# Performance work log

Hardware: AMD Instinct MI355X
Metric: run time of the kernel (lower is better)

## Reference

```python
import jax, jax.numpy as jnp
import numpy as np

EPS = 1e-5

def layer_norm(x, gamma, beta):
    m = jnp.mean(x, axis=-1, keepdims=True)
    v = jnp.var(x, axis=-1, keepdims=True)
    return (x - m) * jax.lax.rsqrt(v + EPS) * gamma + beta


def setup_inputs() -> dict:
    key = jax.random.key(0)
    ks = jax.random.split(key, 8)
    B, N, E, C = 1, 512, 128, 128
    s = 0.02
    inp = {
        "pair_rep": jax.random.normal(ks[0], (B, N, N, E), dtype=jnp.float32),
        "ln_pair_g": jnp.ones((E,), jnp.float32),
        "ln_pair_b": jnp.zeros((E,), jnp.float32),
        "ga_w": jax.random.normal(ks[1], (E, C), jnp.float32) * s,
        "ga_b": jnp.zeros((C,), jnp.float32),
        "la_w": jax.random.normal(ks[2], (E, C), jnp.float32) * s,
        "la_b": jnp.zeros((C,), jnp.float32),
        "gb_w": jax.random.normal(ks[3], (E, C), jnp.float32) * s,
        "gb_b": jnp.zeros((C,), jnp.float32),
        "lb_w": jax.random.normal(ks[4], (E, C), jnp.float32) * s,
        "lb_b": jnp.zeros((C,), jnp.float32),
        "g_w": jax.random.normal(ks[5], (E, E), jnp.float32) * s,
        "g_b": jnp.zeros((E,), jnp.float32),
        "ln_up_g": jnp.ones((C,), jnp.float32),
        "ln_up_b": jnp.zeros((C,), jnp.float32),
        "lu_w": jax.random.normal(ks[6], (C, E), jnp.float32) * s,
        "lu_b": jnp.zeros((E,), jnp.float32),
    }
    return inp


def reference(pair_rep, ln_pair_g, ln_pair_b, ga_w, ga_b, la_w, la_b,
              gb_w, gb_b, lb_w, lb_b, g_w, g_b, ln_up_g, ln_up_b, lu_w, lu_b):
    # pair_rep: [B, N, N, E]
    z = layer_norm(pair_rep, ln_pair_g, ln_pair_b)
    a = jax.nn.sigmoid(z @ ga_w + ga_b) * (z @ la_w + la_b)  # [B,N,N,C]
    b = jax.nn.sigmoid(z @ gb_w + gb_b) * (z @ lb_w + lb_b)  # [B,N,N,C]
    g = jax.nn.sigmoid(z @ g_w + g_b)                        # [B,N,N,E]
    # torch: sum(a.unsqueeze(-3)*b.unsqueeze(-4), dim=-2) == sum_k a[i,k,c]*b[j,k,c]
    update = jnp.einsum("bikc,bjkc->bijc", a, b)             # [B,N,N,C]
    out = g * (layer_norm(update, ln_up_g, ln_up_b) @ lu_w + lu_b)
    return out
```

## Files before the change

kernel.cpp:

```cpp
#include <hip/hip_runtime.h>
#include <hip/hip_bf16.h>

#define NN 512
#define MM (NN*NN)

typedef __attribute__((ext_vector_type(8))) unsigned short u16x8;
typedef __attribute__((ext_vector_type(4))) unsigned short u16x4;
typedef __attribute__((ext_vector_type(8))) __bf16 bf16x8;
typedef __attribute__((ext_vector_type(4))) float f32x4;

static __device__ __forceinline__ unsigned short f2bfi(float f) {
  return __builtin_bit_cast(unsigned short, __float2bfloat16(f));
}
static __device__ __forceinline__ float bf2f(unsigned short h) {
  return __uint_as_float(((unsigned int)h) << 16);
}
static __device__ __forceinline__ bf16x8 ldfrag(const unsigned short* p) {
  u16x8 v = *(const u16x8*)p;
  return __builtin_bit_cast(bf16x8, v);
}
static __device__ __forceinline__ float sigm(float x) {
  return 1.0f / (1.0f + __expf(-x));
}

__global__ void prep_weights(const float* __restrict__ ga_w, const float* __restrict__ la_w,
                             const float* __restrict__ gb_w, const float* __restrict__ lb_w,
                             const float* __restrict__ g_w,  const float* __restrict__ lu_w,
                             unsigned short* __restrict__ WT) {
  int idx = blockIdx.x * 256 + threadIdx.x;
  if (idx >= 768 * 128) return;
  int n = idx >> 7;
  int k = idx & 127;
  int grp = n >> 7, cn = n & 127;
  const float* tabs[6] = {ga_w, la_w, gb_w, lb_w, g_w, lu_w};
  WT[idx] = f2bfi(tabs[grp][k * 128 + cn]);
}

__global__ __launch_bounds__(512, 4) void k1_proj(
    const float* __restrict__ pair, const float* __restrict__ lng, const float* __restrict__ lnb,
    const unsigned short* __restrict__ WT,
    const float* __restrict__ ga_b, const float* __restrict__ la_b,
    const float* __restrict__ gb_b, const float* __restrict__ lb_b,
    const float* __restrict__ g_b,
    unsigned short* __restrict__ a_t, unsigned short* __restrict__ b_t,
    unsigned short* __restrict__ g_buf) {
  __shared__ __align__(16) unsigned short W0[128 * 136];
  __shared__ __align__(16) unsigned short W1[128 * 136];
  const int t = threadIdx.x;
  const size_t m0 = (size_t)blockIdx.x * 128;
  const int wave = t >> 6, lane = t & 63, lrow = lane & 15, qk = lane >> 4;
  const int rbase = t >> 4, off_ = (t & 15) * 8;

  u16x8 rga[4], rla[4], rgb[4], rlb[4], rg[4];
  auto stage_ld = [&](u16x8* r, int base) {
#pragma unroll
    for (int it = 0; it < 4; ++it)
      r[it] = *(const u16x8*)(WT + (size_t)(base + it * 32 + rbase) * 128 + off_);
  };
  auto stage_st = [&](unsigned short* buf, const u16x8* r) {
#pragma unroll
    for (int it = 0; it < 4; ++it)
      *(u16x8*)(buf + (it * 32 + rbase) * 136 + off_) = r[it];
  };

  stage_ld(rga, 0);
  stage_ld(rla, 128);

  {
    const int row = t >> 2, q = t & 3;
    const float* pr = pair + (m0 + row) * 128 + q * 32;
    float vals[32];
    float s = 0.f, ss = 0.f;
#pragma unroll
    for (int it = 0; it < 8; ++it) {
      f32x4 v = *(const f32x4*)(pr + it * 4);
#pragma unroll
      for (int j = 0; j < 4; ++j) { float x = v[j]; vals[it * 4 + j] = x; s += x; ss += x * x; }
    }
    s += __shfl_xor(s, 1);  s += __shfl_xor(s, 2);
    ss += __shfl_xor(ss, 1); ss += __shfl_xor(ss, 2);
    const float mean = s * (1.f / 128.f);
    const float var  = ss * (1.f / 128.f) - mean * mean;
    const float rstd = rsqrtf(var + 1e-5f);
#pragma unroll
    for (int i = 0; i < 4; ++i) {
      u16x8 pk;
#pragma unroll
      for (int j = 0; j < 8; ++j) {
        int c = q * 32 + i * 8 + j;
        pk[j] = f2bfi((vals[i * 8 + j] - mean) * rstd * lng[c] + lnb[c]);
      }
      *(u16x8*)(W0 + row * 136 + q * 32 + i * 8) = pk;
    }
  }
  __syncthreads();

  bf16x8 af[4];
  f32x4 accg[8], accl[8];
  auto run_gemm = [&](const unsigned short* buf, f32x4* acc) {
#pragma unroll
    for (int nt = 0; nt < 8; ++nt)
#pragma unroll
      for (int r = 0; r < 4; ++r) acc[nt][r] = 0.f;
#pragma unroll
    for (int ks = 0; ks < 4; ++ks)
#pragma unroll
      for (int nt = 0; nt < 8; ++nt) {
        bf16x8 bv = ldfrag(buf + (nt * 16 + lrow) * 136 + ks * 32 + 8 * qk);
        acc[nt] = __builtin_amdgcn_mfma_f32_16x16x32_bf16(af[ks], bv, acc[nt], 0, 0, 0);
      }
  };
  auto epi_ab = [&](unsigned short* buf, const float* gbias, const float* lbias) {
#pragma unroll
    for (int nt = 0; nt < 8; ++nt) {
      int col = nt * 16 + lrow;
      float bg = gbias[col], bl = lbias[col];
      u16x4 pk;
#pragma unroll
      for (int r = 0; r < 4; ++r)
        pk[r] = f2bfi(sigm(accg[nt][r] + bg) * (accl[nt][r] + bl));
      *(u16x4*)(buf + col * 136 + wave * 16 + qk * 4) = pk;
    }
  };
  auto wout = [&](unsigned short* dst, const unsigned short* buf) {
#pragma unroll
    for (int it = 0; it < 4; ++it) {
      int idx = it * 512 + t;
      int col = idx >> 4, i = idx & 15;
      *(u16x8*)(dst + (size_t)col * MM + m0 + i * 8) = *(const u16x8*)(buf + col * 136 + i * 8);
    }
  };

#pragma unroll
  for (int ks = 0; ks < 4; ++ks)
    af[ks] = ldfrag(W0 + (wave * 16 + lrow) * 136 + ks * 32 + 8 * qk);
  stage_st(W1, rga);
  stage_ld(rgb, 256);
  __syncthreads();
  run_gemm(W1, accg);
  stage_st(W0, rla);
  stage_ld(rlb, 384);
  __syncthreads();
  run_gemm(W0, accl);
  stage_st(W1, rgb);
  stage_ld(rg, 512);
  __syncthreads();
  epi_ab(W0, ga_b, la_b);
  __syncthreads();
  wout(a_t, W0);
  run_gemm(W1, accg);
  __syncthreads();
  stage_st(W0, rlb);
  stage_st(W1, rg);
  __syncthreads();
  run_gemm(W0, accl);
  __syncthreads();
  epi_ab(W0, gb_b, lb_b);
  run_gemm(W1, accg);
  __syncthreads();
  wout(b_t, W0);
#pragma unroll
  for (int nt = 0; nt < 8; ++nt) {
    int col = nt * 16 + lrow;
    float bg = g_b[col];
#pragma unroll
    for (int r = 0; r < 4; ++r)
      g_buf[(m0 + wave * 16 + qk * 4 + r) * 128 + col] = f2bfi(sigm(accg[nt][r] + bg));
  }
}

__global__ __launch_bounds__(256) void k2_einsum(
    const unsigned short* __restrict__ a_t, const unsigned short* __restrict__ b_t,
    unsigned short* __restrict__ up_t) {
  __shared__ __align__(16) unsigned short sA[2][128 * 40];
  __shared__ __align__(16) unsigned short sB[2][128 * 40];
  const int t = threadIdx.x;
  const int wid = (blockIdx.x & 7) * 256 + (blockIdx.x >> 3);
  const int c = wid >> 4;
  const int i0 = ((wid >> 2) & 3) * 128, j0 = (wid & 3) * 128;
  const unsigned short* Ag = a_t + (size_t)c * MM + (size_t)i0 * 512;
  const unsigned short* Bg = b_t + (size_t)c * MM + (size_t)j0 * 512;
  const int wave = t >> 6, lane = t & 63, wr = wave >> 1, wc = wave & 1;
  const int lrow = lane & 15, qk = lane >> 4;
  const int srow = t >> 2, sq = t & 3;
  f32x4 acc[4][4];
#pragma unroll
  for (int i = 0; i < 4; ++i)
#pragma unroll
    for (int j = 0; j < 4; ++j)
#pragma unroll
      for (int r = 0; r < 4; ++r) acc[i][j][r] = 0.f;

  u16x8 ra[2], rb[2];
  auto tile_ld = [&](int k0) {
#pragma unroll
    for (int h = 0; h < 2; ++h) {
      int row = h * 64 + srow;
      ra[h] = *(const u16x8*)(Ag + (size_t)row * 512 + k0 + sq * 8);
      rb[h] = *(const u16x8*)(Bg + (size_t)row * 512 + k0 + sq * 8);
    }
  };
  auto tile_st = [&](int buf) {
#pragma unroll
    for (int h = 0; h < 2; ++h) {
      int row = h * 64 + srow;
      *(u16x8*)(sA[buf] + row * 40 + sq * 8) = ra[h];
      *(u16x8*)(sB[buf] + row * 40 + sq * 8) = rb[h];
    }
  };

  tile_ld(0);
  tile_st(0);
  __syncthreads();
  int cur = 0;
  for (int ks = 0; ks < 16; ++ks) {
    if (ks < 15) tile_ld((ks + 1) * 32);
    bf16x8 afr[4], bv[4];
#pragma unroll
    for (int mt = 0; mt < 4; ++mt)
      afr[mt] = ldfrag(sA[cur] + (wr * 64 + mt * 16 + lrow) * 40 + 8 * qk);
#pragma unroll
    for (int nt = 0; nt < 4; ++nt)
      bv[nt] = ldfrag(sB[cur] + (wc * 64 + nt * 16 + lrow) * 40 + 8 * qk);
#pragma unroll
    for (int mt = 0; mt < 4; ++mt)
#pragma unroll
      for (int nt = 0; nt < 4; ++nt)
        acc[mt][nt] = __builtin_amdgcn_mfma_f32_16x16x32_bf16(afr[mt], bv[nt], acc[mt][nt], 0, 0, 0);
    if (ks < 15) tile_st(cur ^ 1);
    __syncthreads();
    cur ^= 1;
  }
  unsigned short* up = up_t + (size_t)c * MM;
#pragma unroll
  for (int mt = 0; mt < 4; ++mt)
#pragma unroll
    for (int nt = 0; nt < 4; ++nt) {
      int col = j0 + wc * 64 + nt * 16 + lrow;
#pragma unroll
      for (int r = 0; r < 4; ++r) {
        int row = i0 + wr * 64 + mt * 16 + qk * 4 + r;
        up[(size_t)row * 512 + col] = f2bfi(acc[mt][nt][r]);
      }
    }
}

__global__ __launch_bounds__(256) void k3_final(
    const unsigned short* __restrict__ up_t, const unsigned short* __restrict__ g_buf,
    const unsigned short* __restrict__ WT,
    const float* __restrict__ lnug, const float* __restrict__ lnub,
    const float* __restrict__ lu_b, float* __restrict__ out) {
  __shared__ __align__(16) unsigned short sU[64 * 138];
  __shared__ __align__(16) unsigned short sA[64 * 136];
  __shared__ __align__(16) unsigned short sB[128 * 136];
  const int t = threadIdx.x;
  const size_t m0 = (size_t)blockIdx.x * 64;
#pragma unroll
  for (int it = 0; it < 4; ++it) {
    int idx = it * 256 + t;
    int c = idx >> 3, m8 = (idx & 7) * 8;
    u16x8 v = *(const u16x8*)(up_t + (size_t)c * MM + m0 + m8);
#pragma unroll
    for (int j = 0; j < 8; ++j) sU[(m8 + j) * 138 + c] = v[j];
  }
#pragma unroll
  for (int it = 0; it < 8; ++it) {
    int idx = it * 256 + t;
    int n = idx >> 4, off = (idx & 15) * 8;
    *(u16x8*)(sB + n * 136 + off) = *(const u16x8*)(WT + (size_t)(640 + n) * 128 + off);
  }
  __syncthreads();
  {
    const int row = t >> 2, q = t & 3;
    float vals[32]; float s = 0.f, ss = 0.f;
#pragma unroll
    for (int jj = 0; jj < 32; ++jj) {
      int cc = q + jj * 4;
      float x = bf2f(sU[row * 138 + cc]);
      vals[jj] = x; s += x; ss += x * x;
    }
    s += __shfl_xor(s, 1);  s += __shfl_xor(s, 2);
    ss += __shfl_xor(ss, 1); ss += __shfl_xor(ss, 2);
    float mean = s * (1.f / 128.f);
    float var  = ss * (1.f / 128.f) - mean * mean;
    float rstd = rsqrtf(var + 1e-5f);
#pragma unroll
    for (int jj = 0; jj < 32; ++jj) {
      int cc = q + jj * 4;
      float zn = (vals[jj] - mean) * rstd * lnug[cc] + lnub[cc];
      sA[row * 136 + cc] = f2bfi(zn);
    }
  }
  __syncthreads();
  const int wave = t >> 6, lane = t & 63, lrow = lane & 15, qk = lane >> 4;
  f32x4 acc[8];
#pragma unroll
  for (int i = 0; i < 8; ++i)
#pragma unroll
    for (int r = 0; r < 4; ++r) acc[i][r] = 0.f;
#pragma unroll
  for (int ks = 0; ks < 4; ++ks) {
    int k0 = ks * 32;
    bf16x8 af = ldfrag(sA + (wave * 16 + lrow) * 136 + k0 + 8 * qk);
#pragma unroll
    for (int nt = 0; nt < 8; ++nt) {
      bf16x8 bv = ldfrag(sB + (nt * 16 + lrow) * 136 + k0 + 8 * qk);
      acc[nt] = __builtin_amdgcn_mfma_f32_16x16x32_bf16(af, bv, acc[nt], 0, 0, 0);
    }
  }
#pragma unroll
  for (int nt = 0; nt < 8; ++nt) {
    int e = nt * 16 + lrow;
    float bb = lu_b[e];
#pragma unroll
    for (int r = 0; r < 4; ++r) {
      size_t m = m0 + wave * 16 + qk * 4 + r;
      float lin = acc[nt][r] + bb;
      float gv = bf2f(g_buf[m * 128 + e]);
      out[m * 128 + e] = gv * lin;
    }
  }
}

extern "C" void kernel_launch(void* const* d_in, const int* in_sizes, int n_in,
                              void* d_out, int out_size, void* d_ws, size_t ws_size,
                              hipStream_t stream) {
  const float* pair = (const float*)d_in[0];
  const float* lng  = (const float*)d_in[1];
  const float* lnb  = (const float*)d_in[2];
  const float* ga_w = (const float*)d_in[3];
  const float* ga_b = (const float*)d_in[4];
  const float* la_w = (const float*)d_in[5];
  const float* la_b = (const float*)d_in[6];
  const float* gb_w = (const float*)d_in[7];
  const float* gb_b = (const float*)d_in[8];
  const float* lb_w = (const float*)d_in[9];
  const float* lb_b = (const float*)d_in[10];
  const float* g_w  = (const float*)d_in[11];
  const float* g_b  = (const float*)d_in[12];
  const float* lnug = (const float*)d_in[13];
  const float* lnub = (const float*)d_in[14];
  const float* lu_w = (const float*)d_in[15];
  const float* lu_b = (const float*)d_in[16];
  float* out = (float*)d_out;

  char* ws = (char*)d_ws;
  unsigned short* WT    = (unsigned short*)(ws);
  unsigned short* a_t   = (unsigned short*)(ws + 196608ull);
  unsigned short* b_t   = (unsigned short*)(ws + 67305472ull);
  unsigned short* g_buf = (unsigned short*)(ws + 134414336ull);
  unsigned short* up_t  = (unsigned short*)(ws + 201523200ull);

  hipLaunchKernelGGL(prep_weights, dim3(384), dim3(256), 0, stream,
                     ga_w, la_w, gb_w, lb_w, g_w, lu_w, WT);
  hipLaunchKernelGGL(k1_proj, dim3(2048), dim3(512), 0, stream,
                     pair, lng, lnb, WT, ga_b, la_b, gb_b, lb_b, g_b, a_t, b_t, g_buf);
  hipLaunchKernelGGL(k2_einsum, dim3(2048), dim3(256), 0, stream, a_t, b_t, up_t);
  hipLaunchKernelGGL(k3_final, dim3(4096), dim3(256), 0, stream,
                     up_t, g_buf, WT, lnug, lnub, lu_b, out);
}
```

Baseline: 297.7 us.

## Split layernorm into its own kernel, pre-swizzle weights, enlarge einsum tiles

The pair layernorm moves out of the projection kernel into a separate k0_ln kernel. That kernel writes z in MFMA fragment order so the projection kernel can load A fragments straight from global memory. Projection weights are pre-packed into fragment-linear layout, the a/b output staging in LDS uses an XOR swizzle, and g is written through LDS with coalesced stores. The einsum kernel moves to 256x256 tiles per 512-thread block to get more reuse per LDS load. Nontemporal loads and stores are added throughout, and the up buffer reuses the z buffer. The extra kernel costs an added z write and read through HBM, and the larger einsum tiles may reduce occupancy.

After: 528.3 us. 77.4% more time.

```diff
diff --git a/kernel.cpp b/kernel.cpp
--- a/kernel.cpp
+++ b/kernel.cpp
@@ -26,78 +26,86 @@
 __global__ void prep_weights(const float* __restrict__ ga_w, const float* __restrict__ la_w,
                              const float* __restrict__ gb_w, const float* __restrict__ lb_w,
                              const float* __restrict__ g_w,  const float* __restrict__ lu_w,
-                             unsigned short* __restrict__ WT) {
+                             unsigned short* __restrict__ WT_lu, unsigned short* __restrict__ WF) {
   int idx = blockIdx.x * 256 + threadIdx.x;
-  if (idx >= 768 * 128) return;
-  int n = idx >> 7;
-  int k = idx & 127;
-  int grp = n >> 7, cn = n & 127;
-  const float* tabs[6] = {ga_w, la_w, gb_w, lb_w, g_w, lu_w};
-  WT[idx] = f2bfi(tabs[grp][k * 128 + cn]);
-}
-
-__global__ __launch_bounds__(512, 4) void k1_proj(
+  if (idx < 16384) {
+    int n = idx >> 7, k = idx & 127;
+    WT_lu[idx] = f2bfi(lu_w[k * 128 + n]);
+  } else {
+    int id2 = idx - 16384;
+    int j = id2 & 7, lane = (id2 >> 3) & 63, ks = (id2 >> 9) & 3, nt = (id2 >> 11) & 7, gm = id2 >> 14;
+    int col = nt * 16 + (lane & 15);
+    int k = ks * 32 + (lane >> 4) * 8 + j;
+    const float* tabs[5] = {ga_w, la_w, gb_w, lb_w, g_w};
+    WF[id2] = f2bfi(tabs[gm][k * 128 + col]);
+  }
+}
+
+__global__ __launch_bounds__(512) void k0_ln(
     const float* __restrict__ pair, const float* __restrict__ lng, const float* __restrict__ lnb,
-    const unsigned short* __restrict__ WT,
+    unsigned short* __restrict__ z_g) {
+  const int t = threadIdx.x;
+  const size_t m0 = (size_t)blockIdx.x * 128;
+  const int row = t >> 2, q = t & 3;
+  const float* pr = pair + (m0 + row) * 128 + q * 32;
+  float vals[32];
+  float s = 0.f, ss = 0.f;
+#pragma unroll
+  for (int it = 0; it < 8; ++it) {
+    f32x4 v = __builtin_nontemporal_load((const f32x4*)(pr + it * 4));
+#pragma unroll
+    for (int j = 0; j < 4; ++j) { float x = v[j]; vals[it * 4 + j] = x; s += x; ss += x * x; }
+  }
+  s += __shfl_xor(s, 1);  s += __shfl_xor(s, 2);
+  ss += __shfl_xor(ss, 1); ss += __shfl_xor(ss, 2);
+  const float mean = s * (1.f / 128.f);
+  const float var  = ss * (1.f / 128.f) - mean * mean;
+  const float rstd = rsqrtf(var + 1e-5f);
+  unsigned short* zt = z_g + (size_t)blockIdx.x * 16384 + (row >> 4) * 2048 + q * 512 + (row & 15) * 8;
+#pragma unroll
+  for (int o = 0; o < 4; ++o) {
+    u16x8 pk;
+#pragma unroll
+    for (int j = 0; j < 8; ++j) {
+      int c = q * 32 + o * 8 + j;
+      pk[j] = f2bfi((vals[o * 8 + j] - mean) * rstd * lng[c] + lnb[c]);
+    }
+    __builtin_nontemporal_store(pk, (u16x8*)(zt + o * 128));
+  }
+}
+
+__global__ __launch_bounds__(512, 4) void k1_proj5(
+    const unsigned short* __restrict__ z_g, const unsigned short* __restrict__ WF,
     const float* __restrict__ ga_b, const float* __restrict__ la_b,
     const float* __restrict__ gb_b, const float* __restrict__ lb_b,
     const float* __restrict__ g_b,
     unsigned short* __restrict__ a_t, unsigned short* __restrict__ b_t,
     unsigned short* __restrict__ g_buf) {
-  __shared__ __align__(16) unsigned short W0[128 * 136];
-  __shared__ __align__(16) unsigned short W1[128 * 136];
+  __shared__ __align__(16) unsigned short sW[2][16384];
   const int t = threadIdx.x;
   const size_t m0 = (size_t)blockIdx.x * 128;
   const int wave = t >> 6, lane = t & 63, lrow = lane & 15, qk = lane >> 4;
-  const int rbase = t >> 4, off_ = (t & 15) * 8;
-
-  u16x8 rga[4], rla[4], rgb[4], rlb[4], rg[4];
-  auto stage_ld = [&](u16x8* r, int base) {
-#pragma unroll
-    for (int it = 0; it < 4; ++it)
-      r[it] = *(const u16x8*)(WT + (size_t)(base + it * 32 + rbase) * 128 + off_);
-  };
-  auto stage_st = [&](unsigned short* buf, const u16x8* r) {
-#pragma unroll
-    for (int it = 0; it < 4; ++it)
-      *(u16x8*)(buf + (it * 32 + rbase) * 136 + off_) = r[it];
-  };
-
-  stage_ld(rga, 0);
-  stage_ld(rla, 128);
-
-  {
-    const int row = t >> 2, q = t & 3;
-    const float* pr = pair + (m0 + row) * 128 + q * 32;
-    float vals[32];
-    float s = 0.f, ss = 0.f;
-#pragma unroll
-    for (int it = 0; it < 8; ++it) {
-      f32x4 v = *(const f32x4*)(pr + it * 4);
-#pragma unroll
-      for (int j = 0; j < 4; ++j) { float x = v[j]; vals[it * 4 + j] = x; s += x; ss += x * x; }
-    }
-    s += __shfl_xor(s, 1);  s += __shfl_xor(s, 2);
-    ss += __shfl_xor(ss, 1); ss += __shfl_xor(ss, 2);
-    const float mean = s * (1.f / 128.f);
-    const float var  = ss * (1.f / 128.f) - mean * mean;
-    const float rstd = rsqrtf(var + 1e-5f);
-#pragma unroll
-    for (int i = 0; i < 4; ++i) {
-      u16x8 pk;
-#pragma unroll
-      for (int j = 0; j < 8; ++j) {
-        int c = q * 32 + i * 8 + j;
-        pk[j] = f2bfi((vals[i * 8 + j] - mean) * rstd * lng[c] + lnb[c]);
-      }
-      *(u16x8*)(W0 + row * 136 + q * 32 + i * 8) = pk;
-    }
-  }
-  __syncthreads();
-
+
+  const u16x8* zp = (const u16x8*)z_g + ((size_t)blockIdx.x * 8 + wave) * 256 + lane;
   bf16x8 af[4];
+#pragma unroll
+  for (int ks = 0; ks < 4; ++ks)
+    af[ks] = __builtin_bit_cast(bf16x8, __builtin_nontemporal_load(zp + ks * 64));
+
+  u16x8 r0[4], r1[4];
+  auto stage_ld = [&](u16x8* r, int gm) {
+    const u16x8* src = (const u16x8*)WF + gm * 2048 + t;
+#pragma unroll
+    for (int rr = 0; rr < 4; ++rr) r[rr] = src[rr * 512];
+  };
+  auto stage_st = [&](int buf, const u16x8* r) {
+    u16x8* d = (u16x8*)sW[buf] + t;
+#pragma unroll
+    for (int rr = 0; rr < 4; ++rr) d[rr * 512] = r[rr];
+  };
+
   f32x4 accg[8], accl[8];
-  auto run_gemm = [&](const unsigned short* buf, f32x4* acc) {
+  auto run_gemm = [&](int buf, f32x4* acc) {
 #pragma unroll
     for (int nt = 0; nt < 8; ++nt)
 #pragma unroll
@@ -106,11 +114,13 @@
     for (int ks = 0; ks < 4; ++ks)
 #pragma unroll
       for (int nt = 0; nt < 8; ++nt) {
-        bf16x8 bv = ldfrag(buf + (nt * 16 + lrow) * 136 + ks * 32 + 8 * qk);
+        bf16x8 bv = ldfrag(sW[buf] + ((nt * 4 + ks) * 64 + lane) * 8);
         acc[nt] = __builtin_amdgcn_mfma_f32_16x16x32_bf16(af[ks], bv, acc[nt], 0, 0, 0);
       }
   };
-  auto epi_ab = [&](unsigned short* buf, const float* gbias, const float* lbias) {
+  auto epi_ab = [&](int buf, const float* gbias, const float* lbias) {
+    char* st = (char*)sW[buf];
+    const int rbyte = (wave * 16 + qk * 4) * 2;
 #pragma unroll
     for (int nt = 0; nt < 8; ++nt) {
       int col = nt * 16 + lrow;
@@ -119,73 +129,84 @@
 #pragma unroll
       for (int r = 0; r < 4; ++r)
         pk[r] = f2bfi(sigm(accg[nt][r] + bg) * (accl[nt][r] + bl));
-      *(u16x4*)(buf + col * 136 + wave * 16 + qk * 4) = pk;
-    }
-  };
-  auto wout = [&](unsigned short* dst, const unsigned short* buf) {
+      *(u16x4*)(st + col * 256 + (rbyte ^ ((col & 7) << 5))) = pk;
+    }
+  };
+  auto wout = [&](unsigned short* dst, int buf) {
+    const char* st = (const char*)sW[buf];
 #pragma unroll
     for (int it = 0; it < 4; ++it) {
       int idx = it * 512 + t;
       int col = idx >> 4, i = idx & 15;
-      *(u16x8*)(dst + (size_t)col * MM + m0 + i * 8) = *(const u16x8*)(buf + col * 136 + i * 8);
-    }
-  };
-
-#pragma unroll
-  for (int ks = 0; ks < 4; ++ks)
-    af[ks] = ldfrag(W0 + (wave * 16 + lrow) * 136 + ks * 32 + 8 * qk);
-  stage_st(W1, rga);
-  stage_ld(rgb, 256);
-  __syncthreads();
-  run_gemm(W1, accg);
-  stage_st(W0, rla);
-  stage_ld(rlb, 384);
-  __syncthreads();
-  run_gemm(W0, accl);
-  stage_st(W1, rgb);
-  stage_ld(rg, 512);
-  __syncthreads();
-  epi_ab(W0, ga_b, la_b);
-  __syncthreads();
-  wout(a_t, W0);
-  run_gemm(W1, accg);
-  __syncthreads();
-  stage_st(W0, rlb);
-  stage_st(W1, rg);
-  __syncthreads();
-  run_gemm(W0, accl);
-  __syncthreads();
-  epi_ab(W0, gb_b, lb_b);
-  run_gemm(W1, accg);
-  __syncthreads();
-  wout(b_t, W0);
-#pragma unroll
-  for (int nt = 0; nt < 8; ++nt) {
-    int col = nt * 16 + lrow;
-    float bg = g_b[col];
-#pragma unroll
-    for (int r = 0; r < 4; ++r)
-      g_buf[(m0 + wave * 16 + qk * 4 + r) * 128 + col] = f2bfi(sigm(accg[nt][r] + bg));
-  }
-}
-
-__global__ __launch_bounds__(256) void k2_einsum(
+      u16x8 v = *(const u16x8*)(st + col * 256 + ((i * 16) ^ ((col & 7) << 5)));
+      __builtin_nontemporal_store(v, (u16x8*)(dst + (size_t)col * MM + m0 + i * 8));
+    }
+  };
+
+  stage_ld(r0, 0);
+  stage_ld(r1, 1);
+  stage_st(0, r0);
+  stage_st(1, r1);
+  stage_ld(r0, 2);
+  __syncthreads();
+  run_gemm(0, accg);
+  run_gemm(1, accl);
+  stage_ld(r1, 3);
+  __syncthreads();
+  stage_st(1, r0);
+  epi_ab(0, ga_b, la_b);
+  stage_ld(r0, 4);
+  __syncthreads();
+  wout(a_t, 0);
+  run_gemm(1, accg);
+  __syncthreads();
+  stage_st(0, r1);
+  __syncthreads();
+  run_gemm(0, accl);
+  __syncthreads();
+  epi_ab(0, gb_b, lb_b);
+  stage_st(1, r0);
+  __syncthreads();
+  wout(b_t, 0);
+  run_gemm(1, accg);
+  __syncthreads();
+  {
+    unsigned short* gs = &sW[0][0];
+#pragma unroll
+    for (int nt = 0; nt < 8; ++nt) {
+      int col = nt * 16 + lrow;
+      float bg = g_b[col];
+#pragma unroll
+      for (int r = 0; r < 4; ++r)
+        gs[(wave * 16 + qk * 4 + r) * 136 + col] = f2bfi(sigm(accg[nt][r] + bg));
+    }
+    __syncthreads();
+#pragma unroll
+    for (int it = 0; it < 4; ++it) {
+      int idx = it * 512 + t;
+      int mr = idx >> 4, off = (idx & 15) * 8;
+      u16x8 v = *(const u16x8*)(gs + mr * 136 + off);
+      __builtin_nontemporal_store(v, (u16x8*)(g_buf + (m0 + mr) * 128 + off));
+    }
+  }
+}
+
+__global__ __launch_bounds__(512, 4) void k2_einsum(
     const unsigned short* __restrict__ a_t, const unsigned short* __restrict__ b_t,
     unsigned short* __restrict__ up_t) {
-  __shared__ __align__(16) unsigned short sA[2][128 * 40];
-  __shared__ __align__(16) unsigned short sB[2][128 * 40];
+  __shared__ __align__(16) unsigned short sA[2][256 * 34];
+  __shared__ __align__(16) unsigned short sB[2][256 * 34];
   const int t = threadIdx.x;
-  const int wid = (blockIdx.x & 7) * 256 + (blockIdx.x >> 3);
-  const int c = wid >> 4;
-  const int i0 = ((wid >> 2) & 3) * 128, j0 = (wid & 3) * 128;
+  const int wid = (blockIdx.x & 7) * 64 + (blockIdx.x >> 3);
+  const int c = wid >> 2;
+  const int i0 = ((wid >> 1) & 1) * 256, j0 = (wid & 1) * 256;
   const unsigned short* Ag = a_t + (size_t)c * MM + (size_t)i0 * 512;
   const unsigned short* Bg = b_t + (size_t)c * MM + (size_t)j0 * 512;
-  const int wave = t >> 6, lane = t & 63, wr = wave >> 1, wc = wave & 1;
+  const int wave = t >> 6, lane = t & 63, wr = wave >> 2, wc = wave & 3;
   const int lrow = lane & 15, qk = lane >> 4;
-  const int srow = t >> 2, sq = t & 3;
-  f32x4 acc[4][4];
-#pragma unroll
-  for (int i = 0; i < 4; ++i)
+  f32x4 acc[8][4];
+#pragma unroll
+  for (int i = 0; i < 8; ++i)
 #pragma unroll
     for (int j = 0; j < 4; ++j)
 #pragma unroll
@@ -195,17 +216,19 @@
   auto tile_ld = [&](int k0) {
 #pragma unroll
     for (int h = 0; h < 2; ++h) {
-      int row = h * 64 + srow;
-      ra[h] = *(const u16x8*)(Ag + (size_t)row * 512 + k0 + sq * 8);
-      rb[h] = *(const u16x8*)(Bg + (size_t)row * 512 + k0 + sq * 8);
+      int idx = h * 512 + t;
+      int row = idx >> 2, qq = idx & 3;
+      ra[h] = *(const u16x8*)(Ag + (size_t)row * 512 + k0 + qq * 8);
+      rb[h] = *(const u16x8*)(Bg + (size_t)row * 512 + k0 + qq * 8);
     }
   };
   auto tile_st = [&](int buf) {
 #pragma unroll
     for (int h = 0; h < 2; ++h) {
-      int row = h * 64 + srow;
-      *(u16x8*)(sA[buf] + row * 40 + sq * 8) = ra[h];
-      *(u16x8*)(sB[buf] + row * 40 + sq * 8) = rb[h];
+      int idx = h * 512 + t;
+      int row = idx >> 2, qq = idx & 3;
+      *(u16x8*)(sA[buf] + row * 34 + qq * 8) = ra[h];
+      *(u16x8*)(sB[buf] + row * 34 + qq * 8) = rb[h];
     }
   };
 
@@ -215,15 +238,15 @@
   int cur = 0;
   for (int ks = 0; ks < 16; ++ks) {
     if (ks < 15) tile_ld((ks + 1) * 32);
-    bf16x8 afr[4], bv[4];
-#pragma unroll
-    for (int mt = 0; mt < 4; ++mt)
-      afr[mt] = ldfrag(sA[cur] + (wr * 64 + mt * 16 + lrow) * 40 + 8 * qk);
+    bf16x8 afr[8], bv[4];
+#pragma unroll
+    for (int mt = 0; mt < 8; ++mt)
+      afr[mt] = ldfrag(sA[cur] + (wr * 128 + mt * 16 + lrow) * 34 + qk * 8);
 #pragma unroll
     for (int nt = 0; nt < 4; ++nt)
-      bv[nt] = ldfrag(sB[cur] + (wc * 64 + nt * 16 + lrow) * 40 + 8 * qk);
-#pragma unroll
-    for (int mt = 0; mt < 4; ++mt)
+      bv[nt] = ldfrag(sB[cur] + (wc * 64 + nt * 16 + lrow) * 34 + qk * 8);
+#pragma unroll
+    for (int mt = 0; mt < 8; ++mt)
 #pragma unroll
       for (int nt = 0; nt < 4; ++nt)
         acc[mt][nt] = __builtin_amdgcn_mfma_f32_16x16x32_bf16(afr[mt], bv[nt], acc[mt][nt], 0, 0, 0);
@@ -233,13 +256,13 @@
   }
   unsigned short* up = up_t + (size_t)c * MM;
 #pragma unroll
-  for (int mt = 0; mt < 4; ++mt)
+  for (int mt = 0; mt < 8; ++mt)
 #pragma unroll
     for (int nt = 0; nt < 4; ++nt) {
       int col = j0 + wc * 64 + nt * 16 + lrow;
 #pragma unroll
       for (int r = 0; r < 4; ++r) {
-        int row = i0 + wr * 64 + mt * 16 + qk * 4 + r;
+        int row = i0 + wr * 128 + mt * 16 + qk * 4 + r;
         up[(size_t)row * 512 + col] = f2bfi(acc[mt][nt][r]);
       }
     }
@@ -247,7 +270,7 @@
 
 __global__ __launch_bounds__(256) void k3_final(
     const unsigned short* __restrict__ up_t, const unsigned short* __restrict__ g_buf,
-    const unsigned short* __restrict__ WT,
+    const unsigned short* __restrict__ WT_lu,
     const float* __restrict__ lnug, const float* __restrict__ lnub,
     const float* __restrict__ lu_b, float* __restrict__ out) {
   __shared__ __align__(16) unsigned short sU[64 * 138];
@@ -259,7 +282,7 @@
   for (int it = 0; it < 4; ++it) {
     int idx = it * 256 + t;
     int c = idx >> 3, m8 = (idx & 7) * 8;
-    u16x8 v = *(const u16x8*)(up_t + (size_t)c * MM + m0 + m8);
+    u16x8 v = __builtin_nontemporal_load((const u16x8*)(up_t + (size_t)c * MM + m0 + m8));
 #pragma unroll
     for (int j = 0; j < 8; ++j) sU[(m8 + j) * 138 + c] = v[j];
   }
@@ -267,7 +290,7 @@
   for (int it = 0; it < 8; ++it) {
     int idx = it * 256 + t;
     int n = idx >> 4, off = (idx & 15) * 8;
-    *(u16x8*)(sB + n * 136 + off) = *(const u16x8*)(WT + (size_t)(640 + n) * 128 + off);
+    *(u16x8*)(sB + n * 136 + off) = *(const u16x8*)(WT_lu + (size_t)n * 128 + off);
   }
   __syncthreads();
   {
@@ -345,17 +368,19 @@
   float* out = (float*)d_out;
 
   char* ws = (char*)d_ws;
-  unsigned short* WT    = (unsigned short*)(ws);
-  unsigned short* a_t   = (unsigned short*)(ws + 196608ull);
-  unsigned short* b_t   = (unsigned short*)(ws + 67305472ull);
-  unsigned short* g_buf = (unsigned short*)(ws + 134414336ull);
-  unsigned short* up_t  = (unsigned short*)(ws + 201523200ull);
+  unsigned short* WT_lu = (unsigned short*)(ws);
+  unsigned short* WF    = (unsigned short*)(ws + 32768ull);
+  unsigned short* zup   = (unsigned short*)(ws + 196608ull);
+  unsigned short* a_t   = (unsigned short*)(ws + 67305472ull);
+  unsigned short* b_t   = (unsigned short*)(ws + 134414336ull);
+  unsigned short* g_buf = (unsigned short*)(ws + 201523200ull);
 
   hipLaunchKernelGGL(prep_weights, dim3(384), dim3(256), 0, stream,
-                     ga_w, la_w, gb_w, lb_w, g_w, lu_w, WT);
-  hipLaunchKernelGGL(k1_proj, dim3(2048), dim3(512), 0, stream,
-                     pair, lng, lnb, WT, ga_b, la_b, gb_b, lb_b, g_b, a_t, b_t, g_buf);
-  hipLaunchKernelGGL(k2_einsum, dim3(2048), dim3(256), 0, stream, a_t, b_t, up_t);
+                     ga_w, la_w, gb_w, lb_w, g_w, lu_w, WT_lu, WF);
+  hipLaunchKernelGGL(k0_ln, dim3(2048), dim3(512), 0, stream, pair, lng, lnb, zup);
+  hipLaunchKernelGGL(k1_proj5, dim3(2048), dim3(512), 0, stream,
+                     zup, WF, ga_b, la_b, gb_b, lb_b, g_b, a_t, b_t, g_buf);
+  hipLaunchKernelGGL(k2_einsum, dim3(512), dim3(512), 0, stream, a_t, b_t, zup);
   hipLaunchKernelGGL(k3_final, dim3(4096), dim3(256), 0, stream,
-                     up_t, g_buf, WT, lnug, lnub, lu_b, out);
-}
+                     zup, g_buf, WT_lu, lnug, lnub, lu_b, out);
+}
```
